# Optimization experiments

Measured on AMD Instinct MI355X. Metric: run time of the kernel, lower is better.

The kernel has to match this reference:

```python
import jax, jax.numpy as jnp
import numpy as np

L, H, P = 131072, 128, 128
STEP_RESCALE = 1.0
CONJ_SYM = True


def setup_inputs() -> dict:
    key = jax.random.key(0)
    ks = jax.random.split(key, 9)
    x = jax.random.normal(ks[0], (L, H), jnp.float32)
    # stable SSM: real parts of Lambda must be negative so |dA| < 1
    A_real_log = -(0.5 + jax.random.uniform(ks[1], (P,), jnp.float32))
    A_imag = 3.0 * jax.random.normal(ks[2], (P,), jnp.float32)
    B_re = jax.random.normal(ks[3], (P, H), jnp.float32) / np.sqrt(H)
    B_im = jax.random.normal(ks[4], (P, H), jnp.float32) / np.sqrt(H)
    C_re = jax.random.normal(ks[5], (H, P), jnp.float32) / np.sqrt(P)
    C_im = jax.random.normal(ks[6], (H, P), jnp.float32) / np.sqrt(P)
    D = jax.random.normal(ks[7], (H,), jnp.float32)
    # softplus(inv_dt) small -> small timestep dt
    inv_dt = jax.random.normal(ks[8], (P,), jnp.float32) - 4.0
    return {"x": x, "A_real_log": A_real_log, "A_imag": A_imag,
            "B_re": B_re, "B_im": B_im, "C_re": C_re, "C_im": C_im,
            "D": D, "inv_dt": inv_dt}


def reference(x, A_real_log, A_imag, B_re, B_im, C_re, C_im, D, inv_dt):
    # A = Lambda (diagonal complex state matrix), shape (P,)
    A = A_real_log + 1j * A_imag
    dt = STEP_RESCALE * jax.nn.softplus(inv_dt)            # (P,)
    # bilinear (Tustin) discretization
    BL = 1.0 / (1.0 - 0.5 * dt * A)                        # (P,)
    dA = BL * (1.0 + 0.5 * dt * A)                         # (P,)
    B = B_re + 1j * B_im                                   # (P,H)
    dB = (BL * dt)[:, None] * B                            # (P,H)
    # input projection into state space: (L,P) complex
    Bu = jnp.einsum('lh,ph->lp', x + 0j, dB)
    # linear recurrence h_k = dA * h_{k-1} + Bu_k via parallel associative scan
    A_elems = jnp.broadcast_to(dA[None, :], Bu.shape)
    def binop(q1, q2):
        a1, b1 = q1
        a2, b2 = q2
        return a1 * a2, a2 * b1 + b2
    _, hs = jax.lax.associative_scan(binop, (A_elems, Bu), axis=0)  # (L,P)
    C = C_re + 1j * C_im                                   # (H,P)
    y = jnp.einsum('lp,hp->lh', hs, C).real                # (L,H)
    if CONJ_SYM:
        y = 2.0 * y
    return y + x * D[None, :]
```

## Files before the change

kernel.cpp:

```cpp
#include <hip/hip_runtime.h>

#define L_LEN 131072
#define H_DIM 128
#define P_DIM 128
#define SEG 32
#define NSEG (L_LEN / SEG)
#define ROWS 64
#define NBLK (L_LEN / ROWS)

typedef unsigned int uint32;
typedef unsigned short u16;
typedef short bf16x8 __attribute__((ext_vector_type(8)));
typedef float f32x4 __attribute__((ext_vector_type(4)));

constexpr size_t OFF_HL  = 0;
constexpr size_t N_HLF   = (size_t)L_LEN * 256 / 2;
constexpr size_t OFF_DA  = OFF_HL + N_HLF;
constexpr size_t OFF_SC  = OFF_DA + 256;
constexpr size_t OFF_POW = OFF_SC + 256;
constexpr size_t OFF_E   = OFF_POW + 32 * 256;
constexpr size_t OFF_HIN = OFF_E + (size_t)NSEG * 256;
constexpr size_t OFF_W1F = OFF_HIN + (size_t)NSEG * 256;
constexpr size_t OFF_W2F = OFF_W1F + 32768;

__device__ __forceinline__ u16 f2bf(float v) {
    uint32 u = __builtin_bit_cast(uint32, v);
    uint32 r = u + 0x7FFFu + ((u >> 16) & 1u);
    return (u16)(r >> 16);
}
__device__ __forceinline__ float bf2f(u16 h) {
    uint32 u = ((uint32)h) << 16;
    return __builtin_bit_cast(float, u);
}
__device__ __forceinline__ uint32 cvtpk(float lo, float hi) {
    uint32 r;
    asm("v_cvt_pk_bf16_f32 %0, %1, %2" : "=v"(r) : "v"(lo), "v"(hi));
    return r;
}
__device__ __forceinline__ float2 cfma(float2 a, float2 h, float2 c) {
    float2 r;
    r.x = fmaf(a.x, h.x, fmaf(-a.y, h.y, c.x));
    r.y = fmaf(a.x, h.y, fmaf(a.y, h.x, c.y));
    return r;
}
__device__ __forceinline__ float2 cmul(float2 a, float2 b) {
    return make_float2(fmaf(a.x, b.x, -a.y * b.y), fmaf(a.x, b.y, a.y * b.x));
}
__device__ __forceinline__ float2 unpk(uint32 w) {
    return make_float2(bf2f((u16)(w & 0xffffu)), bf2f((u16)(w >> 16)));
}
__device__ __forceinline__ bf16x8 fixup(uint4 hl, f32x4 d0, f32x4 d1, f32x4 h0, f32x4 h1) {
    float2 c0 = cfma(make_float2(d0[0], d0[1]), make_float2(h0[0], h0[1]), unpk(hl.x));
    float2 c1 = cfma(make_float2(d0[2], d0[3]), make_float2(h0[2], h0[3]), unpk(hl.y));
    float2 c2 = cfma(make_float2(d1[0], d1[1]), make_float2(h1[0], h1[1]), unpk(hl.z));
    float2 c3 = cfma(make_float2(d1[2], d1[3]), make_float2(h1[2], h1[3]), unpk(hl.w));
    union { uint32 u[4]; bf16x8 v; } r;
    r.u[0] = cvtpk(c0.x, c0.y); r.u[1] = cvtpk(c1.x, c1.y);
    r.u[2] = cvtpk(c2.x, c2.y); r.u[3] = cvtpk(c3.x, c3.y);
    return r.v;
}

__global__ void k0a(const float* __restrict__ Arl, const float* __restrict__ Ai,
                    const float* __restrict__ invdt,
                    float* __restrict__ dA, float* __restrict__ sc,
                    float* __restrict__ dApow) {
    int p = threadIdx.x;
    if (p >= P_DIM) return;
    float idt = invdt[p];
    float dt = (idt > 20.f) ? idt : log1pf(expf(idt));
    float ar = Arl[p], ai = Ai[p];
    float zr = 0.5f * dt * ar, zi = 0.5f * dt * ai;
    float dr = 1.f - zr, di = -zi;
    float inv = 1.f / (dr * dr + di * di);
    float blr = dr * inv, bli = -di * inv;
    float nr = 1.f + zr, ni = zi;
    float2 a = make_float2(fmaf(blr, nr, -bli * ni), fmaf(blr, ni, bli * nr));
    dA[2 * p] = a.x; dA[2 * p + 1] = a.y;
    sc[2 * p] = blr * dt; sc[2 * p + 1] = bli * dt;
    float2 pw = a;
    for (int i = 0; i < SEG; ++i) {
        dApow[((size_t)i * P_DIM + p) * 2]     = pw.x;
        dApow[((size_t)i * P_DIM + p) * 2 + 1] = pw.y;
        pw = cmul(pw, a);
    }
}

__global__ void k0b(const float* __restrict__ Bre, const float* __restrict__ Bim,
                    const float* __restrict__ Cre, const float* __restrict__ Cim,
                    const float* __restrict__ sc,
                    u16* __restrict__ W1F, u16* __restrict__ W2F) {
    int tid = blockIdx.x * 256 + threadIdx.x;
    int lane = tid & 63;
    int fb = (tid >> 6) & 63;
    int ar = lane & 15, aq = lane >> 4;
    ushort4 hiA, hiB, loA, loB;
    u16* dst;
    if (tid < 4096) {
        int kt = fb >> 4, cf = fb & 15;
        int q = cf * 16 + ar;
        int p = q >> 1, c = q & 1;
        int h0 = kt * 32 + aq * 8;
        float2 s = ((const float2*)sc)[p];
        u16 hh[8], ll[8];
        #pragma unroll
        for (int j = 0; j < 8; ++j) {
            float br = Bre[p * H_DIM + h0 + j], bi = Bim[p * H_DIM + h0 + j];
            float re = fmaf(s.x, br, -s.y * bi);
            float im = fmaf(s.x, bi,  s.y * br);
            float v = c ? im : re;
            u16 h = f2bf(v); hh[j] = h; ll[j] = f2bf(v - bf2f(h));
        }
        hiA = make_ushort4(hh[0], hh[1], hh[2], hh[3]);
        hiB = make_ushort4(hh[4], hh[5], hh[6], hh[7]);
        loA = make_ushort4(ll[0], ll[1], ll[2], ll[3]);
        loB = make_ushort4(ll[4], ll[5], ll[6], ll[7]);
        dst = W1F + fb * 1024 + lane * 8;
    } else {
        int kk = fb >> 3, cf = fb & 7;
        int h = cf * 16 + ar;
        int q0 = kk * 32 + aq * 8;
        u16 hh[8], ll[8];
        #pragma unroll
        for (int j = 0; j < 8; ++j) {
            int q = q0 + j; int p = q >> 1;
            float v = (q & 1) ? (-2.f * Cim[h * P_DIM + p]) : (2.f * Cre[h * P_DIM + p]);
            u16 hv = f2bf(v); hh[j] = hv; ll[j] = f2bf(v - bf2f(hv));
        }
        hiA = make_ushort4(hh[0], hh[1], hh[2], hh[3]);
        hiB = make_ushort4(hh[4], hh[5], hh[6], hh[7]);
        loA = make_ushort4(ll[0], ll[1], ll[2], ll[3]);
        loB = make_ushort4(ll[4], ll[5], ll[6], ll[7]);
        dst = W2F + fb * 1024 + lane * 8;
    }
    *(ushort4*)(dst)       = hiA;
    *(ushort4*)(dst + 4)   = hiB;
    *(ushort4*)(dst + 512) = loA;
    *(ushort4*)(dst + 516) = loB;
}

__global__ __launch_bounds__(256) void k1(const float* __restrict__ x,
                                          const u16* __restrict__ W1F,
                                          const float* __restrict__ dA,
                                          u16* __restrict__ HL,
                                          float* __restrict__ E) {
    __shared__ __align__(16) char smem[32768];
    u16* As_hi = (u16*)smem;
    u16* SB    = (u16*)smem;
    int t = threadIdx.x, lane = t & 63, wid = t >> 6;
    size_t l0 = (size_t)blockIdx.x * ROWS;
    int ar = lane & 15, aq = lane >> 4, ak = aq * 8;

    bf16x8 bhp[4][4];
    #pragma unroll
    for (int kt = 0; kt < 4; ++kt)
        #pragma unroll
        for (int nf = 0; nf < 4; ++nf)
            bhp[kt][nf] = *(const bf16x8*)(W1F + (size_t)(kt * 16 + wid * 4 + nf) * 1024 + lane * 8);

    float4 xv[8];
    #pragma unroll
    for (int j = 0; j < 8; ++j) {
        int f = j * 256 + t; int row = f >> 5, c4 = f & 31;
        xv[j] = *(const float4*)(x + (l0 + row) * H_DIM + c4 * 4);
    }
    #pragma unroll
    for (int j = 0; j < 8; ++j) {
        int f = j * 256 + t; int row = f >> 5, c4 = f & 31;
        uint2 wv;
        wv.x = cvtpk(xv[j].x, xv[j].y);
        wv.y = cvtpk(xv[j].z, xv[j].w);
        *(uint2*)&As_hi[row * 136 + c4 * 4] = wv;
    }
    __syncthreads();

    f32x4 acc[4][4];
    #pragma unroll
    for (int a = 0; a < 4; ++a)
        #pragma unroll
        for (int b = 0; b < 4; ++b) acc[a][b] = (f32x4)0.f;

    #pragma unroll
    for (int kt = 0; kt < 4; ++kt) {
        bf16x8 ah[4];
        #pragma unroll
        for (int mf = 0; mf < 4; ++mf) {
            int row = mf * 16 + ar;
            ah[mf] = *(const bf16x8*)&As_hi[row * 136 + kt * 32 + ak];
        }
        #pragma unroll
        for (int nf = 0; nf < 4; ++nf)
            #pragma unroll
            for (int mf = 0; mf < 4; ++mf)
                acc[mf][nf] = __builtin_amdgcn_mfma_f32_16x16x32_bf16(ah[mf], bhp[kt][nf], acc[mf][nf], 0, 0, 0);
    }
    __syncthreads();

    int sr = aq * 4;
    #pragma unroll
    for (int mf = 0; mf < 4; ++mf)
        #pragma unroll
        for (int nf = 0; nf < 4; ++nf) {
            int col = wid * 64 + nf * 16 + ar;
            uint32 w01 = cvtpk(acc[mf][nf][0], acc[mf][nf][1]);
            uint32 w23 = cvtpk(acc[mf][nf][2], acc[mf][nf][3]);
            int r0 = mf * 16 + sr;
            SB[(r0 + 0) * 256 + (((col >> 3) ^ ((r0 + 0) & 7)) << 3) + (col & 7)] = (u16)w01;
            SB[(r0 + 1) * 256 + (((col >> 3) ^ ((r0 + 1) & 7)) << 3) + (col & 7)] = (u16)(w01 >> 16);
            SB[(r0 + 2) * 256 + (((col >> 3) ^ ((r0 + 2) & 7)) << 3) + (col & 7)] = (u16)w23;
            SB[(r0 + 3) * 256 + (((col >> 3) ^ ((r0 + 3) & 7)) << 3) + (col & 7)] = (u16)(w23 >> 16);
        }
    __syncthreads();

    {
        int s = t >> 7, p = t & 127;
        float2 a = ((const float2*)dA)[p];
        uint32 buf[SEG];
        #pragma unroll
        for (int i = 0; i < SEG; ++i) {
            int row = s * 32 + i;
            buf[i] = *(const uint32*)&SB[row * 256 + (((p >> 2) ^ (row & 7)) << 3) + (p & 3) * 2];
        }
        float2 h = make_float2(0.f, 0.f);
        #pragma unroll
        for (int i = 0; i < SEG; ++i) {
            h = cfma(a, h, unpk(buf[i]));
            buf[i] = cvtpk(h.x, h.y);
        }
        #pragma unroll
        for (int i = 0; i < SEG; ++i) {
            int row = s * 32 + i;
            *(uint32*)&SB[row * 256 + (((p >> 2) ^ (row & 7)) << 3) + (p & 3) * 2] = buf[i];
        }
        ((float2*)E)[((size_t)blockIdx.x * 2 + s) * P_DIM + p] = h;
    }
    __syncthreads();

    #pragma unroll
    for (int j = 0; j < 8; ++j) {
        int f = j * 256 + t; int row = f >> 5, blk = f & 31;
        uint4 v = *(const uint4*)&SB[row * 256 + ((blk ^ (row & 7)) << 3)];
        *(uint4*)(HL + (l0 + row) * 256 + blk * 8) = v;
    }
}

__global__ __launch_bounds__(256) void k3(const float* __restrict__ E,
                                          const float* __restrict__ dA,
                                          float* __restrict__ Hin) {
    __shared__ float4 s0[256], s1[256];
    int m = blockIdx.x, j = threadIdx.x;
    float2 aS = ((const float2*)dA)[m];
    #pragma unroll
    for (int i = 0; i < 5; ++i) aS = cmul(aS, aS);
    const float2* e = (const float2*)E;
    float2 ebuf[16];
    #pragma unroll
    for (int i = 0; i < 16; ++i) ebuf[i] = e[(size_t)(j * 16 + i) * P_DIM + m];
    float2 B = ebuf[0];
    #pragma unroll
    for (int i = 1; i < 16; ++i) B = cfma(aS, B, ebuf[i]);
    float2 A = aS;
    #pragma unroll
    for (int i = 0; i < 4; ++i) A = cmul(A, A);
    s0[j] = make_float4(A.x, A.y, B.x, B.y);
    __syncthreads();
    float4 *src = s0, *dst = s1;
    for (int d = 1; d < 256; d <<= 1) {
        float4 v = src[j];
        if (j >= d) {
            float4 u = src[j - d];
            float2 uA = make_float2(u.x, u.y), uB = make_float2(u.z, u.w);
            float2 vA = make_float2(v.x, v.y), vB = make_float2(v.z, v.w);
            float2 nA = cmul(uA, vA);
            float2 nB = cfma(vA, uB, vB);
            v = make_float4(nA.x, nA.y, nB.x, nB.y);
        }
        dst[j] = v;
        __syncthreads();
        float4* tmp = src; src = dst; dst = tmp;
    }
    float2 pre = make_float2(0.f, 0.f);
    if (j > 0) { float4 u = src[j - 1]; pre = make_float2(u.z, u.w); }
    float2* hin = (float2*)Hin;
    #pragma unroll
    for (int i = 0; i < 16; ++i) {
        hin[(size_t)(j * 16 + i) * P_DIM + m] = pre;
        pre = cfma(aS, pre, ebuf[i]);
    }
}

__global__ __launch_bounds__(256) void k4(const float* __restrict__ x,
                                          const u16* __restrict__ HL,
                                          const u16* __restrict__ W2F,
                                          const float* __restrict__ dApow,
                                          const float* __restrict__ Hin,
                                          const float* __restrict__ Dv,
                                          float* __restrict__ y) {
    __shared__ __align__(16) char smem[34816];
    u16*   SB   = (u16*)smem;
    float* HinS = (float*)(smem + 32768);
    float* SBF  = (float*)smem;
    int t = threadIdx.x, lane = t & 63, wid = t >> 6;
    size_t l0 = (size_t)blockIdx.x * ROWS;

    bf16x8 bhp[8][2];
    #pragma unroll
    for (int kk = 0; kk < 8; ++kk)
        #pragma unroll
        for (int nf = 0; nf < 2; ++nf)
            bhp[kk][nf] = *(const bf16x8*)(W2F + (size_t)(kk * 8 + wid * 2 + nf) * 1024 + lane * 8);

    ((float2*)HinS)[t] = ((const float2*)Hin)[(size_t)blockIdx.x * 2 * P_DIM + t];
    __syncthreads();

    uint4 va[8];
    #pragma unroll
    for (int j = 0; j < 8; ++j) {
        int f = j * 256 + t; int row = f >> 5, blk = f & 31;
        va[j] = *(const uint4*)(HL + (l0 + row) * 256 + blk * 8);
    }
    f32x4 da[8][2];
    #pragma unroll
    for (int j = 0; j < 8; ++j) {
        int f = j * 256 + t; int row = f >> 5, blk = f & 31;
        const float* dp = dApow + (size_t)(row & 31) * 256 + blk * 8;
        da[j][0] = *(const f32x4*)dp;
        da[j][1] = *(const f32x4*)(dp + 4);
    }
    #pragma unroll
    for (int j = 0; j < 8; ++j) {
        int f = j * 256 + t; int row = f >> 5, blk = f & 31;
        int sg = row >> 5;
        f32x4 h0 = *(const f32x4*)&HinS[sg * 256 + blk * 8];
        f32x4 h1 = *(const f32x4*)&HinS[sg * 256 + blk * 8 + 4];
        bf16x8 o = fixup(va[j], da[j][0], da[j][1], h0, h1);
        *(bf16x8*)&SB[row * 256 + ((blk ^ (row & 7)) << 3)] = o;
    }
    __syncthreads();

    f32x4 acc[4][2];
    #pragma unroll
    for (int a = 0; a < 4; ++a)
        #pragma unroll
        for (int b = 0; b < 2; ++b) acc[a][b] = (f32x4)0.f;
    int ar = lane & 15, aq = lane >> 4;
    #pragma unroll
    for (int kk = 0; kk < 8; ++kk) {
        bf16x8 af[4];
        #pragma unroll
        for (int mf = 0; mf < 4; ++mf) {
            int row = mf * 16 + ar;
            int blk = kk * 4 + aq;
            af[mf] = *(const bf16x8*)&SB[row * 256 + ((blk ^ (row & 7)) << 3)];
        }
        #pragma unroll
        for (int nf = 0; nf < 2; ++nf)
            #pragma unroll
            for (int mf = 0; mf < 4; ++mf)
                acc[mf][nf] = __builtin_amdgcn_mfma_f32_16x16x32_bf16(af[mf], bhp[kk][nf], acc[mf][nf], 0, 0, 0);
    }
    __syncthreads();

    int sr = aq * 4;
    #pragma unroll
    for (int mf = 0; mf < 4; ++mf)
        #pragma unroll
        for (int nf = 0; nf < 2; ++nf)
            #pragma unroll
            for (int r = 0; r < 4; ++r) {
                int row = mf * 16 + sr + r;
                int col = wid * 32 + nf * 16 + ar;
                SBF[row * 130 + col] = acc[mf][nf][r];
            }
    __syncthreads();

    int c4 = t & 31;
    float4 dv = *(const float4*)(Dv + c4 * 4);
    #pragma unroll
    for (int j = 0; j < 8; ++j) {
        int row = j * 8 + (t >> 5);
        float4 sv = *(float4*)&SBF[row * 130 + c4 * 4];
        float4 xv = *(const float4*)(x + (l0 + row) * H_DIM + c4 * 4);
        float4 out;
        out.x = fmaf(xv.x, dv.x, sv.x);
        out.y = fmaf(xv.y, dv.y, sv.y);
        out.z = fmaf(xv.z, dv.z, sv.z);
        out.w = fmaf(xv.w, dv.w, sv.w);
        *(float4*)(y + (l0 + row) * H_DIM + c4 * 4) = out;
    }
}

extern "C" void kernel_launch(void* const* d_in, const int* in_sizes, int n_in,
                              void* d_out, int out_size, void* d_ws, size_t ws_size,
                              hipStream_t stream) {
    const float* x     = (const float*)d_in[0];
    const float* Arl   = (const float*)d_in[1];
    const float* Ai    = (const float*)d_in[2];
    const float* Bre   = (const float*)d_in[3];
    const float* Bim   = (const float*)d_in[4];
    const float* Cre   = (const float*)d_in[5];
    const float* Cim   = (const float*)d_in[6];
    const float* Dv    = (const float*)d_in[7];
    const float* invdt = (const float*)d_in[8];
    float* y  = (float*)d_out;
    float* ws = (float*)d_ws;

    u16* hl  = (u16*)(ws + OFF_HL);
    u16* w1f = (u16*)(ws + OFF_W1F);
    u16* w2f = (u16*)(ws + OFF_W2F);

    k0a<<<1, 128, 0, stream>>>(Arl, Ai, invdt, ws + OFF_DA, ws + OFF_SC, ws + OFF_POW);
    k0b<<<32, 256, 0, stream>>>(Bre, Bim, Cre, Cim, ws + OFF_SC, w1f, w2f);
    k1<<<NBLK, 256, 0, stream>>>(x, w1f, ws + OFF_DA, hl, ws + OFF_E);
    k3<<<128, 256, 0, stream>>>(ws + OFF_E, ws + OFF_DA, ws + OFF_HIN);
    k4<<<NBLK, 256, 0, stream>>>(x, hl, w2f, ws + OFF_POW,
                                 ws + OFF_HIN, Dv, y);
}
```

Measured before the change: 89.55 us.

## Make k1 and k4 process several row tiles per block with register prefetch

k1 and k4 now each loop over four 64-row tiles per block, so the grid shrinks fourfold. Weight fragments (and dA powers in k4) are loaded into registers once per block and reused across tiles. The next tile's x or HL data and Hin values are prefetched into registers or a double-buffered shared array while the current tile's MFMA work runs. The cost is fewer blocks for latency hiding (2048 to 512), one extra barrier per tile, and higher register pressure from the prefetch buffers.

```diff
diff --git a/kernel.cpp b/kernel.cpp
--- a/kernel.cpp
+++ b/kernel.cpp
@@ -7,6 +7,8 @@
 #define NSEG (L_LEN / SEG)
 #define ROWS 64
 #define NBLK (L_LEN / ROWS)
+#define ITERS 4
+#define PBLK (NBLK / ITERS)
 
 typedef unsigned int uint32;
 typedef unsigned short u16;
@@ -147,8 +149,8 @@
     u16* As_hi = (u16*)smem;
     u16* SB    = (u16*)smem;
     int t = threadIdx.x, lane = t & 63, wid = t >> 6;
-    size_t l0 = (size_t)blockIdx.x * ROWS;
     int ar = lane & 15, aq = lane >> 4, ak = aq * 8;
+    int rb0 = blockIdx.x * ITERS;
 
     bf16x8 bhp[4][4];
     #pragma unroll
@@ -161,85 +163,95 @@
     #pragma unroll
     for (int j = 0; j < 8; ++j) {
         int f = j * 256 + t; int row = f >> 5, c4 = f & 31;
-        xv[j] = *(const float4*)(x + (l0 + row) * H_DIM + c4 * 4);
-    }
-    #pragma unroll
-    for (int j = 0; j < 8; ++j) {
-        int f = j * 256 + t; int row = f >> 5, c4 = f & 31;
-        uint2 wv;
-        wv.x = cvtpk(xv[j].x, xv[j].y);
-        wv.y = cvtpk(xv[j].z, xv[j].w);
-        *(uint2*)&As_hi[row * 136 + c4 * 4] = wv;
-    }
-    __syncthreads();
-
-    f32x4 acc[4][4];
-    #pragma unroll
-    for (int a = 0; a < 4; ++a)
-        #pragma unroll
-        for (int b = 0; b < 4; ++b) acc[a][b] = (f32x4)0.f;
-
-    #pragma unroll
-    for (int kt = 0; kt < 4; ++kt) {
-        bf16x8 ah[4];
-        #pragma unroll
-        for (int mf = 0; mf < 4; ++mf) {
-            int row = mf * 16 + ar;
-            ah[mf] = *(const bf16x8*)&As_hi[row * 136 + kt * 32 + ak];
-        }
-        #pragma unroll
-        for (int nf = 0; nf < 4; ++nf)
+        xv[j] = *(const float4*)(x + ((size_t)rb0 * ROWS + row) * H_DIM + c4 * 4);
+    }
+
+    for (int it = 0; it < ITERS; ++it) {
+        size_t l0 = (size_t)(rb0 + it) * ROWS;
+        #pragma unroll
+        for (int j = 0; j < 8; ++j) {
+            int f = j * 256 + t; int row = f >> 5, c4 = f & 31;
+            uint2 wv;
+            wv.x = cvtpk(xv[j].x, xv[j].y);
+            wv.y = cvtpk(xv[j].z, xv[j].w);
+            *(uint2*)&As_hi[row * 136 + c4 * 4] = wv;
+        }
+        __syncthreads();
+
+        if (it + 1 < ITERS) {
+            #pragma unroll
+            for (int j = 0; j < 8; ++j) {
+                int f = j * 256 + t; int row = f >> 5, c4 = f & 31;
+                xv[j] = *(const float4*)(x + (l0 + ROWS + row) * H_DIM + c4 * 4);
+            }
+        }
+
+        f32x4 acc[4][4];
+        #pragma unroll
+        for (int a = 0; a < 4; ++a)
+            #pragma unroll
+            for (int b = 0; b < 4; ++b) acc[a][b] = (f32x4)0.f;
+        #pragma unroll
+        for (int kt = 0; kt < 4; ++kt) {
+            bf16x8 ah[4];
             #pragma unroll
             for (int mf = 0; mf < 4; ++mf)
-                acc[mf][nf] = __builtin_amdgcn_mfma_f32_16x16x32_bf16(ah[mf], bhp[kt][nf], acc[mf][nf], 0, 0, 0);
-    }
-    __syncthreads();
-
-    int sr = aq * 4;
-    #pragma unroll
-    for (int mf = 0; mf < 4; ++mf)
-        #pragma unroll
-        for (int nf = 0; nf < 4; ++nf) {
-            int col = wid * 64 + nf * 16 + ar;
-            uint32 w01 = cvtpk(acc[mf][nf][0], acc[mf][nf][1]);
-            uint32 w23 = cvtpk(acc[mf][nf][2], acc[mf][nf][3]);
-            int r0 = mf * 16 + sr;
-            SB[(r0 + 0) * 256 + (((col >> 3) ^ ((r0 + 0) & 7)) << 3) + (col & 7)] = (u16)w01;
-            SB[(r0 + 1) * 256 + (((col >> 3) ^ ((r0 + 1) & 7)) << 3) + (col & 7)] = (u16)(w01 >> 16);
-            SB[(r0 + 2) * 256 + (((col >> 3) ^ ((r0 + 2) & 7)) << 3) + (col & 7)] = (u16)w23;
-            SB[(r0 + 3) * 256 + (((col >> 3) ^ ((r0 + 3) & 7)) << 3) + (col & 7)] = (u16)(w23 >> 16);
-        }
-    __syncthreads();
-
-    {
-        int s = t >> 7, p = t & 127;
-        float2 a = ((const float2*)dA)[p];
-        uint32 buf[SEG];
-        #pragma unroll
-        for (int i = 0; i < SEG; ++i) {
-            int row = s * 32 + i;
-            buf[i] = *(const uint32*)&SB[row * 256 + (((p >> 2) ^ (row & 7)) << 3) + (p & 3) * 2];
-        }
-        float2 h = make_float2(0.f, 0.f);
-        #pragma unroll
-        for (int i = 0; i < SEG; ++i) {
-            h = cfma(a, h, unpk(buf[i]));
-            buf[i] = cvtpk(h.x, h.y);
-        }
-        #pragma unroll
-        for (int i = 0; i < SEG; ++i) {
-            int row = s * 32 + i;
-            *(uint32*)&SB[row * 256 + (((p >> 2) ^ (row & 7)) << 3) + (p & 3) * 2] = buf[i];
-        }
-        ((float2*)E)[((size_t)blockIdx.x * 2 + s) * P_DIM + p] = h;
-    }
-    __syncthreads();
-
-    #pragma unroll
-    for (int j = 0; j < 8; ++j) {
-        int f = j * 256 + t; int row = f >> 5, blk = f & 31;
-        uint4 v = *(const uint4*)&SB[row * 256 + ((blk ^ (row & 7)) << 3)];
-        *(uint4*)(HL + (l0 + row) * 256 + blk * 8) = v;
+                ah[mf] = *(const bf16x8*)&As_hi[(mf * 16 + ar) * 136 + kt * 32 + ak];
+            #pragma unroll
+            for (int nf = 0; nf < 4; ++nf)
+                #pragma unroll
+                for (int mf = 0; mf < 4; ++mf)
+                    acc[mf][nf] = __builtin_amdgcn_mfma_f32_16x16x32_bf16(ah[mf], bhp[kt][nf], acc[mf][nf], 0, 0, 0);
+        }
+        __syncthreads();
+
+        int sr = aq * 4;
+        #pragma unroll
+        for (int mf = 0; mf < 4; ++mf)
+            #pragma unroll
+            for (int nf = 0; nf < 4; ++nf) {
+                int col = wid * 64 + nf * 16 + ar;
+                uint32 w01 = cvtpk(acc[mf][nf][0], acc[mf][nf][1]);
+                uint32 w23 = cvtpk(acc[mf][nf][2], acc[mf][nf][3]);
+                int r0 = mf * 16 + sr;
+                SB[(r0 + 0) * 256 + (((col >> 3) ^ ((r0 + 0) & 7)) << 3) + (col & 7)] = (u16)w01;
+                SB[(r0 + 1) * 256 + (((col >> 3) ^ ((r0 + 1) & 7)) << 3) + (col & 7)] = (u16)(w01 >> 16);
+                SB[(r0 + 2) * 256 + (((col >> 3) ^ ((r0 + 2) & 7)) << 3) + (col & 7)] = (u16)w23;
+                SB[(r0 + 3) * 256 + (((col >> 3) ^ ((r0 + 3) & 7)) << 3) + (col & 7)] = (u16)(w23 >> 16);
+            }
+        __syncthreads();
+
+        {
+            int s = t >> 7, p = t & 127;
+            float2 a = ((const float2*)dA)[p];
+            uint32 buf[SEG];
+            #pragma unroll
+            for (int i = 0; i < SEG; ++i) {
+                int row = s * 32 + i;
+                buf[i] = *(const uint32*)&SB[row * 256 + (((p >> 2) ^ (row & 7)) << 3) + (p & 3) * 2];
+            }
+            float2 h = make_float2(0.f, 0.f);
+            #pragma unroll
+            for (int i = 0; i < SEG; ++i) {
+                h = cfma(a, h, unpk(buf[i]));
+                buf[i] = cvtpk(h.x, h.y);
+            }
+            #pragma unroll
+            for (int i = 0; i < SEG; ++i) {
+                int row = s * 32 + i;
+                *(uint32*)&SB[row * 256 + (((p >> 2) ^ (row & 7)) << 3) + (p & 3) * 2] = buf[i];
+            }
+            ((float2*)E)[((size_t)(rb0 + it) * 2 + s) * P_DIM + p] = h;
+        }
+        __syncthreads();
+
+        #pragma unroll
+        for (int j = 0; j < 8; ++j) {
+            int f = j * 256 + t; int row = f >> 5, blk = f & 31;
+            uint4 v = *(const uint4*)&SB[row * 256 + ((blk ^ (row & 7)) << 3)];
+            *(uint4*)(HL + (l0 + row) * 256 + blk * 8) = v;
+        }
+        __syncthreads();
     }
 }
 
@@ -295,12 +307,13 @@
                                           const float* __restrict__ Hin,
                                           const float* __restrict__ Dv,
                                           float* __restrict__ y) {
-    __shared__ __align__(16) char smem[34816];
-    u16*   SB   = (u16*)smem;
-    float* HinS = (float*)(smem + 32768);
-    float* SBF  = (float*)smem;
+    __shared__ __align__(16) char smem[37376];
+    u16*   SB    = (u16*)smem;
+    float* SBF   = (float*)smem;
+    float* HinSA = (float*)(smem + 33280);
+    float* HinSB = (float*)(smem + 35328);
     int t = threadIdx.x, lane = t & 63, wid = t >> 6;
-    size_t l0 = (size_t)blockIdx.x * ROWS;
+    int rb0 = blockIdx.x * ITERS;
 
     bf16x8 bhp[8][2];
     #pragma unroll
@@ -309,15 +322,6 @@
         for (int nf = 0; nf < 2; ++nf)
             bhp[kk][nf] = *(const bf16x8*)(W2F + (size_t)(kk * 8 + wid * 2 + nf) * 1024 + lane * 8);
 
-    ((float2*)HinS)[t] = ((const float2*)Hin)[(size_t)blockIdx.x * 2 * P_DIM + t];
-    __syncthreads();
-
-    uint4 va[8];
-    #pragma unroll
-    for (int j = 0; j < 8; ++j) {
-        int f = j * 256 + t; int row = f >> 5, blk = f & 31;
-        va[j] = *(const uint4*)(HL + (l0 + row) * 256 + blk * 8);
-    }
     f32x4 da[8][2];
     #pragma unroll
     for (int j = 0; j < 8; ++j) {
@@ -326,66 +330,93 @@
         da[j][0] = *(const f32x4*)dp;
         da[j][1] = *(const f32x4*)(dp + 4);
     }
+
+    ((float2*)HinSA)[t] = ((const float2*)Hin)[(size_t)rb0 * 2 * P_DIM + t];
+    uint4 va[8];
     #pragma unroll
     for (int j = 0; j < 8; ++j) {
         int f = j * 256 + t; int row = f >> 5, blk = f & 31;
-        int sg = row >> 5;
-        f32x4 h0 = *(const f32x4*)&HinS[sg * 256 + blk * 8];
-        f32x4 h1 = *(const f32x4*)&HinS[sg * 256 + blk * 8 + 4];
-        bf16x8 o = fixup(va[j], da[j][0], da[j][1], h0, h1);
-        *(bf16x8*)&SB[row * 256 + ((blk ^ (row & 7)) << 3)] = o;
+        va[j] = *(const uint4*)(HL + ((size_t)rb0 * ROWS + row) * 256 + blk * 8);
     }
     __syncthreads();
 
-    f32x4 acc[4][2];
-    #pragma unroll
-    for (int a = 0; a < 4; ++a)
-        #pragma unroll
-        for (int b = 0; b < 2; ++b) acc[a][b] = (f32x4)0.f;
     int ar = lane & 15, aq = lane >> 4;
-    #pragma unroll
-    for (int kk = 0; kk < 8; ++kk) {
-        bf16x8 af[4];
-        #pragma unroll
-        for (int mf = 0; mf < 4; ++mf) {
-            int row = mf * 16 + ar;
-            int blk = kk * 4 + aq;
-            af[mf] = *(const bf16x8*)&SB[row * 256 + ((blk ^ (row & 7)) << 3)];
-        }
-        #pragma unroll
-        for (int nf = 0; nf < 2; ++nf)
-            #pragma unroll
-            for (int mf = 0; mf < 4; ++mf)
-                acc[mf][nf] = __builtin_amdgcn_mfma_f32_16x16x32_bf16(af[mf], bhp[kk][nf], acc[mf][nf], 0, 0, 0);
-    }
-    __syncthreads();
-
-    int sr = aq * 4;
-    #pragma unroll
-    for (int mf = 0; mf < 4; ++mf)
-        #pragma unroll
-        for (int nf = 0; nf < 2; ++nf)
-            #pragma unroll
-            for (int r = 0; r < 4; ++r) {
-                int row = mf * 16 + sr + r;
-                int col = wid * 32 + nf * 16 + ar;
-                SBF[row * 130 + col] = acc[mf][nf][r];
-            }
-    __syncthreads();
-
-    int c4 = t & 31;
-    float4 dv = *(const float4*)(Dv + c4 * 4);
-    #pragma unroll
-    for (int j = 0; j < 8; ++j) {
-        int row = j * 8 + (t >> 5);
-        float4 sv = *(float4*)&SBF[row * 130 + c4 * 4];
-        float4 xv = *(const float4*)(x + (l0 + row) * H_DIM + c4 * 4);
-        float4 out;
-        out.x = fmaf(xv.x, dv.x, sv.x);
-        out.y = fmaf(xv.y, dv.y, sv.y);
-        out.z = fmaf(xv.z, dv.z, sv.z);
-        out.w = fmaf(xv.w, dv.w, sv.w);
-        *(float4*)(y + (l0 + row) * H_DIM + c4 * 4) = out;
+    for (int it = 0; it < ITERS; ++it) {
+        size_t l0 = (size_t)(rb0 + it) * ROWS;
+        float* cur = (it & 1) ? HinSB : HinSA;
+        float* nxt = (it & 1) ? HinSA : HinSB;
+
+        #pragma unroll
+        for (int j = 0; j < 8; ++j) {
+            int f = j * 256 + t; int row = f >> 5, blk = f & 31;
+            int sg = row >> 5;
+            f32x4 h0 = *(const f32x4*)&cur[sg * 256 + blk * 8];
+            f32x4 h1 = *(const f32x4*)&cur[sg * 256 + blk * 8 + 4];
+            bf16x8 o = fixup(va[j], da[j][0], da[j][1], h0, h1);
+            *(bf16x8*)&SB[row * 256 + ((blk ^ (row & 7)) << 3)] = o;
+        }
+        __syncthreads();
+
+        if (it + 1 < ITERS) {
+            #pragma unroll
+            for (int j = 0; j < 8; ++j) {
+                int f = j * 256 + t; int row = f >> 5, blk = f & 31;
+                va[j] = *(const uint4*)(HL + (l0 + ROWS + row) * 256 + blk * 8);
+            }
+        }
+
+        f32x4 acc[4][2];
+        #pragma unroll
+        for (int a = 0; a < 4; ++a)
+            #pragma unroll
+            for (int b = 0; b < 2; ++b) acc[a][b] = (f32x4)0.f;
+        #pragma unroll
+        for (int kk = 0; kk < 8; ++kk) {
+            bf16x8 af[4];
+            #pragma unroll
+            for (int mf = 0; mf < 4; ++mf) {
+                int row = mf * 16 + ar;
+                int blk = kk * 4 + aq;
+                af[mf] = *(const bf16x8*)&SB[row * 256 + ((blk ^ (row & 7)) << 3)];
+            }
+            #pragma unroll
+            for (int nf = 0; nf < 2; ++nf)
+                #pragma unroll
+                for (int mf = 0; mf < 4; ++mf)
+                    acc[mf][nf] = __builtin_amdgcn_mfma_f32_16x16x32_bf16(af[mf], bhp[kk][nf], acc[mf][nf], 0, 0, 0);
+        }
+        __syncthreads();
+
+        int sr = aq * 4;
+        #pragma unroll
+        for (int mf = 0; mf < 4; ++mf)
+            #pragma unroll
+            for (int nf = 0; nf < 2; ++nf)
+                #pragma unroll
+                for (int r = 0; r < 4; ++r) {
+                    int row = mf * 16 + sr + r;
+                    int col = wid * 32 + nf * 16 + ar;
+                    SBF[row * 130 + col] = acc[mf][nf][r];
+                }
+        if (it + 1 < ITERS)
+            ((float2*)nxt)[t] = ((const float2*)Hin)[(size_t)(rb0 + it + 1) * 2 * P_DIM + t];
+        __syncthreads();
+
+        int c4 = t & 31;
+        float4 dv = *(const float4*)(Dv + c4 * 4);
+        #pragma unroll
+        for (int j = 0; j < 8; ++j) {
+            int row = j * 8 + (t >> 5);
+            float4 sv = *(float4*)&SBF[row * 130 + c4 * 4];
+            float4 xv = *(const float4*)(x + (l0 + row) * H_DIM + c4 * 4);
+            float4 out;
+            out.x = fmaf(xv.x, dv.x, sv.x);
+            out.y = fmaf(xv.y, dv.y, sv.y);
+            out.z = fmaf(xv.z, dv.z, sv.z);
+            out.w = fmaf(xv.w, dv.w, sv.w);
+            *(float4*)(y + (l0 + row) * H_DIM + c4 * 4) = out;
+        }
+        __syncthreads();
     }
 }
 
@@ -410,8 +441,8 @@
 
     k0a<<<1, 128, 0, stream>>>(Arl, Ai, invdt, ws + OFF_DA, ws + OFF_SC, ws + OFF_POW);
     k0b<<<32, 256, 0, stream>>>(Bre, Bim, Cre, Cim, ws + OFF_SC, w1f, w2f);
-    k1<<<NBLK, 256, 0, stream>>>(x, w1f, ws + OFF_DA, hl, ws + OFF_E);
+    k1<<<PBLK, 256, 0, stream>>>(x, w1f, ws + OFF_DA, hl, ws + OFF_E);
     k3<<<128, 256, 0, stream>>>(ws + OFF_E, ws + OFF_DA, ws + OFF_HIN);
-    k4<<<NBLK, 256, 0, stream>>>(x, hl, w2f, ws + OFF_POW,
+    k4<<<PBLK, 256, 0, stream>>>(x, hl, w2f, ws + OFF_POW,
                                  ws + OFF_HIN, Dv, y);
 }
```

Measured after the change: 91.64 us. 2.3% more time.

## Fuse setup kernels and use wave-shuffle scan for segment carries

Applied to the files above, without the earlier changes.

Merges the two setup kernels into one launch: each thread recomputes the discretization scale itself, and block 0 also writes dA and its powers. This removes one kernel launch and its dependency gap. The carry-propagation kernel replaces its shared-memory Hillis-Steele scan, which needed 8 block barriers, with an in-wavefront shuffle scan plus a small cross-wave combine through shared memory. The cost is redundant transcendental math in the setup kernel and a serial loop over previous wave aggregates.

```diff
diff --git a/kernel.cpp b/kernel.cpp
--- a/kernel.cpp
+++ b/kernel.cpp
@@ -16,8 +16,7 @@
 constexpr size_t OFF_HL  = 0;
 constexpr size_t N_HLF   = (size_t)L_LEN * 256 / 2;
 constexpr size_t OFF_DA  = OFF_HL + N_HLF;
-constexpr size_t OFF_SC  = OFF_DA + 256;
-constexpr size_t OFF_POW = OFF_SC + 256;
+constexpr size_t OFF_POW = OFF_DA + 256;
 constexpr size_t OFF_E   = OFF_POW + 32 * 256;
 constexpr size_t OFF_HIN = OFF_E + (size_t)NSEG * 256;
 constexpr size_t OFF_W1F = OFF_HIN + (size_t)NSEG * 256;
@@ -60,35 +59,12 @@
     return r.v;
 }
 
-__global__ void k0a(const float* __restrict__ Arl, const float* __restrict__ Ai,
-                    const float* __restrict__ invdt,
-                    float* __restrict__ dA, float* __restrict__ sc,
-                    float* __restrict__ dApow) {
-    int p = threadIdx.x;
-    if (p >= P_DIM) return;
-    float idt = invdt[p];
-    float dt = (idt > 20.f) ? idt : log1pf(expf(idt));
-    float ar = Arl[p], ai = Ai[p];
-    float zr = 0.5f * dt * ar, zi = 0.5f * dt * ai;
-    float dr = 1.f - zr, di = -zi;
-    float inv = 1.f / (dr * dr + di * di);
-    float blr = dr * inv, bli = -di * inv;
-    float nr = 1.f + zr, ni = zi;
-    float2 a = make_float2(fmaf(blr, nr, -bli * ni), fmaf(blr, ni, bli * nr));
-    dA[2 * p] = a.x; dA[2 * p + 1] = a.y;
-    sc[2 * p] = blr * dt; sc[2 * p + 1] = bli * dt;
-    float2 pw = a;
-    for (int i = 0; i < SEG; ++i) {
-        dApow[((size_t)i * P_DIM + p) * 2]     = pw.x;
-        dApow[((size_t)i * P_DIM + p) * 2 + 1] = pw.y;
-        pw = cmul(pw, a);
-    }
-}
-
-__global__ void k0b(const float* __restrict__ Bre, const float* __restrict__ Bim,
-                    const float* __restrict__ Cre, const float* __restrict__ Cim,
-                    const float* __restrict__ sc,
-                    u16* __restrict__ W1F, u16* __restrict__ W2F) {
+__global__ void k0(const float* __restrict__ Arl, const float* __restrict__ Ai,
+                   const float* __restrict__ invdt,
+                   const float* __restrict__ Bre, const float* __restrict__ Bim,
+                   const float* __restrict__ Cre, const float* __restrict__ Cim,
+                   float* __restrict__ dA, float* __restrict__ dApow,
+                   u16* __restrict__ W1F, u16* __restrict__ W2F) {
     int tid = blockIdx.x * 256 + threadIdx.x;
     int lane = tid & 63;
     int fb = (tid >> 6) & 63;
@@ -100,7 +76,14 @@
         int q = cf * 16 + ar;
         int p = q >> 1, c = q & 1;
         int h0 = kt * 32 + aq * 8;
-        float2 s = ((const float2*)sc)[p];
+        float idt = invdt[p];
+        float dt = (idt > 20.f) ? idt : log1pf(expf(idt));
+        float arl = Arl[p], aii = Ai[p];
+        float zr = 0.5f * dt * arl, zi = 0.5f * dt * aii;
+        float drr = 1.f - zr, dii = -zi;
+        float inv = 1.f / (drr * drr + dii * dii);
+        float blr = drr * inv, bli = -dii * inv;
+        float2 s = make_float2(blr * dt, bli * dt);
         u16 hh[8], ll[8];
         #pragma unroll
         for (int j = 0; j < 8; ++j) {
@@ -136,6 +119,26 @@
     *(ushort4*)(dst + 4)   = hiB;
     *(ushort4*)(dst + 512) = loA;
     *(ushort4*)(dst + 516) = loB;
+
+    if (blockIdx.x == 0 && threadIdx.x < 128) {
+        int p = threadIdx.x;
+        float idt = invdt[p];
+        float dt = (idt > 20.f) ? idt : log1pf(expf(idt));
+        float arl = Arl[p], aii = Ai[p];
+        float zr = 0.5f * dt * arl, zi = 0.5f * dt * aii;
+        float drr = 1.f - zr, dii = -zi;
+        float inv = 1.f / (drr * drr + dii * dii);
+        float blr = drr * inv, bli = -dii * inv;
+        float nr = 1.f + zr, ni = zi;
+        float2 a = make_float2(fmaf(blr, nr, -bli * ni), fmaf(blr, ni, bli * nr));
+        dA[2 * p] = a.x; dA[2 * p + 1] = a.y;
+        float2 pw = a;
+        for (int i = 0; i < SEG; ++i) {
+            dApow[((size_t)i * P_DIM + p) * 2]     = pw.x;
+            dApow[((size_t)i * P_DIM + p) * 2 + 1] = pw.y;
+            pw = cmul(pw, a);
+        }
+    }
 }
 
 __global__ __launch_bounds__(256) void k1(const float* __restrict__ x,
@@ -246,44 +249,52 @@
 __global__ __launch_bounds__(256) void k3(const float* __restrict__ E,
                                           const float* __restrict__ dA,
                                           float* __restrict__ Hin) {
-    __shared__ float4 s0[256], s1[256];
-    int m = blockIdx.x, j = threadIdx.x;
+    __shared__ float4 wagg[4];
+    int m = blockIdx.x, t = threadIdx.x;
+    int lane = t & 63, w = t >> 6;
     float2 aS = ((const float2*)dA)[m];
     #pragma unroll
     for (int i = 0; i < 5; ++i) aS = cmul(aS, aS);
     const float2* e = (const float2*)E;
     float2 ebuf[16];
     #pragma unroll
-    for (int i = 0; i < 16; ++i) ebuf[i] = e[(size_t)(j * 16 + i) * P_DIM + m];
-    float2 B = ebuf[0];
-    #pragma unroll
-    for (int i = 1; i < 16; ++i) B = cfma(aS, B, ebuf[i]);
-    float2 A = aS;
-    #pragma unroll
-    for (int i = 0; i < 4; ++i) A = cmul(A, A);
-    s0[j] = make_float4(A.x, A.y, B.x, B.y);
-    __syncthreads();
-    float4 *src = s0, *dst = s1;
-    for (int d = 1; d < 256; d <<= 1) {
-        float4 v = src[j];
-        if (j >= d) {
-            float4 u = src[j - d];
-            float2 uA = make_float2(u.x, u.y), uB = make_float2(u.z, u.w);
-            float2 vA = make_float2(v.x, v.y), vB = make_float2(v.z, v.w);
-            float2 nA = cmul(uA, vA);
-            float2 nB = cfma(vA, uB, vB);
-            v = make_float4(nA.x, nA.y, nB.x, nB.y);
-        }
-        dst[j] = v;
-        __syncthreads();
-        float4* tmp = src; src = dst; dst = tmp;
-    }
-    float2 pre = make_float2(0.f, 0.f);
-    if (j > 0) { float4 u = src[j - 1]; pre = make_float2(u.z, u.w); }
+    for (int i = 0; i < 16; ++i) ebuf[i] = e[(size_t)(t * 16 + i) * P_DIM + m];
+    float2 Bv = ebuf[0];
+    #pragma unroll
+    for (int i = 1; i < 16; ++i) Bv = cfma(aS, Bv, ebuf[i]);
+    float2 Av = aS;
+    #pragma unroll
+    for (int i = 0; i < 4; ++i) Av = cmul(Av, Av);
+
+    #pragma unroll
+    for (int d = 1; d < 64; d <<= 1) {
+        float uAx = __shfl_up(Av.x, (unsigned)d, 64);
+        float uAy = __shfl_up(Av.y, (unsigned)d, 64);
+        float uBx = __shfl_up(Bv.x, (unsigned)d, 64);
+        float uBy = __shfl_up(Bv.y, (unsigned)d, 64);
+        if (lane >= d) {
+            float2 uA = make_float2(uAx, uAy), uB = make_float2(uBx, uBy);
+            Bv = cfma(Av, uB, Bv);
+            Av = cmul(uA, Av);
+        }
+    }
+    if (lane == 63) wagg[w] = make_float4(Av.x, Av.y, Bv.x, Bv.y);
+    __syncthreads();
+    float2 Pb = make_float2(0.f, 0.f);
+    for (int i = 0; i < w; ++i) {
+        float4 u = wagg[i];
+        float2 Wa = make_float2(u.x, u.y), Wb = make_float2(u.z, u.w);
+        Pb = cfma(Wa, Pb, Wb);
+    }
+    float eAx = __shfl_up(Av.x, 1u, 64), eAy = __shfl_up(Av.y, 1u, 64);
+    float eBx = __shfl_up(Bv.x, 1u, 64), eBy = __shfl_up(Bv.y, 1u, 64);
+    float2 eA = make_float2(eAx, eAy), eB = make_float2(eBx, eBy);
+    if (lane == 0) { eA = make_float2(1.f, 0.f); eB = make_float2(0.f, 0.f); }
+    float2 pre = cfma(eA, Pb, eB);
     float2* hin = (float2*)Hin;
     #pragma unroll
     for (int i = 0; i < 16; ++i) {
-        hin[(size_t)(j * 16 + i) * P_DIM + m] = pre;
+        hin[(size_t)(t * 16 + i) * P_DIM + m] = pre;
         pre = cfma(aS, pre, ebuf[i]);
     }
 }
@@ -408,8 +419,8 @@
     u16* w1f = (u16*)(ws + OFF_W1F);
     u16* w2f = (u16*)(ws + OFF_W2F);
 
-    k0a<<<1, 128, 0, stream>>>(Arl, Ai, invdt, ws + OFF_DA, ws + OFF_SC, ws + OFF_POW);
-    k0b<<<32, 256, 0, stream>>>(Bre, Bim, Cre, Cim, ws + OFF_SC, w1f, w2f);
+    k0<<<32, 256, 0, stream>>>(Arl, Ai, invdt, Bre, Bim, Cre, Cim,
+                               ws + OFF_DA, ws + OFF_POW, w1f, w2f);
     k1<<<NBLK, 256, 0, stream>>>(x, w1f, ws + OFF_DA, hl, ws + OFF_E);
     k3<<<128, 256, 0, stream>>>(ws + OFF_E, ws + OFF_DA, ws + OFF_HIN);
     k4<<<NBLK, 256, 0, stream>>>(x, hl, w2f, ws + OFF_POW,
```

Result: faster. 86.43 us (-3.5%).
